# Kernel tuning notes

Hardware: AMD Instinct MI355X
Metric: run time of the kernel (lower is better)

The kernel has to match this reference:

```python
import jax, jax.numpy as jnp
import numpy as np

N = 8192
NFEAT = 512
NHID = 512
NCLASS = 8
EPS = 1e-9
ADJ_P = 0.01  # edge density


def setup_inputs() -> dict:
    key = jax.random.key(0)
    ks = jax.random.split(key, 16)
    adj = (jax.random.uniform(ks[0], (N, N)) < ADJ_P).astype(jnp.float32)
    x = jax.random.normal(ks[1], (N, NFEAT), dtype=jnp.float32)
    s_in = 1.0 / np.sqrt(NFEAT)
    s_h = 1.0 / np.sqrt(NHID)
    return {
        "adj": adj,
        "x": x,
        "gcn1_W": jax.random.normal(ks[2], (NFEAT, NHID), jnp.float32) * s_in,
        "gcn1_b": jnp.zeros((NHID,), jnp.float32),
        "Qw": jax.random.normal(ks[3], (NHID, NHID), jnp.float32) * s_h,
        "Qb": jnp.zeros((NHID,), jnp.float32),
        "Kw": jax.random.normal(ks[4], (NHID, NHID), jnp.float32) * s_h,
        "Kb": jnp.zeros((NHID,), jnp.float32),
        "Vw": jax.random.normal(ks[5], (NHID, NHID), jnp.float32) * s_h,
        "Vb": jnp.zeros((NHID,), jnp.float32),
        "ln_g": jnp.ones((NHID,), jnp.float32),
        "ln_b": jnp.zeros((NHID,), jnp.float32),
        "gcn2_W": jax.random.normal(ks[6], (NHID, NCLASS), jnp.float32) * s_h,
        "gcn2_b": jnp.zeros((NCLASS,), jnp.float32),
    }


def _gcn_norm(a):
    # symmetric degree normalization D^{-1/2} A D^{-1/2}, degrees = row sums
    d_inv_sqrt = jax.lax.rsqrt(a.sum(axis=1) + EPS)  # [N]
    return d_inv_sqrt[:, None] * a * d_inv_sqrt[None, :]


def _layer_norm(x, g, b):
    mu = x.mean(axis=-1, keepdims=True)
    var = x.var(axis=-1, keepdims=True)
    return (x - mu) * jax.lax.rsqrt(var + 1e-5) * g + b


def reference(adj, x, gcn1_W, gcn1_b, Qw, Qb, Kw, Kb, Vw, Vb, ln_g, ln_b, gcn2_W, gcn2_b):
    # GraphConvolution: adj @ (x W) + b, then ReLU
    h = jax.nn.relu(adj @ (x @ gcn1_W) + gcn1_b)  # [N, NHID]
    Qh = h @ Qw + Qb
    Kh = h @ Kw + Kb
    Vh = h @ Vw + Vb
    # adjacency-masked dense scores (multiplicative mask, as in original)
    A_tilde = adj * (Qh @ Kh.T)  # [N, N]
    attention = jax.nn.softmax(A_tilde, axis=1)
    X_tilde = _gcn_norm(attention) @ Vh  # [N, NHID]
    X_tilde = _layer_norm(X_tilde, ln_g, ln_b)
    z = adj @ (X_tilde @ gcn2_W) + gcn2_b  # [N, NCLASS]
    return jax.nn.softmax(z, axis=1)
```

## Files before the change

kernel.cpp:

```cpp
#include <hip/hip_runtime.h>
#include <math.h>

#define N_NODES 8192
#define NFEAT 512
#define NHID 512
#define NCLASS 8
#define RCAP 192
#define KB_SPLIT 1536
#define KA_SPLIT 1024
#define NSLICE 8

__device__ inline ushort f2bf(float f) {
  uint32_t u = __float_as_uint(f);
  uint32_t r = u + 0x7fffu + ((u >> 16) & 1u);
  return (ushort)(r >> 16);
}
__device__ inline float bf2f(ushort h) { return __uint_as_float(((uint32_t)h) << 16); }

__global__ __launch_bounds__(256) void build_ell(const float* __restrict__ adj,
                                                 int* __restrict__ colidx,
                                                 int* __restrict__ deg) {
  int row = blockIdx.x;
  __shared__ int cnt;
  __shared__ int cols[RCAP];
  if (threadIdx.x == 0) cnt = 0;
  __syncthreads();
  const float4* arow = (const float4*)(adj + (size_t)row * N_NODES);
  for (int i = threadIdx.x; i < N_NODES / 4; i += 256) {
    float4 v = arow[i];
    int base = i * 4;
    if (v.x > 0.5f) { int p = atomicAdd(&cnt, 1); if (p < RCAP) cols[p] = base; }
    if (v.y > 0.5f) { int p = atomicAdd(&cnt, 1); if (p < RCAP) cols[p] = base + 1; }
    if (v.z > 0.5f) { int p = atomicAdd(&cnt, 1); if (p < RCAP) cols[p] = base + 2; }
    if (v.w > 0.5f) { int p = atomicAdd(&cnt, 1); if (p < RCAP) cols[p] = base + 3; }
  }
  __syncthreads();
  int d = cnt < RCAP ? cnt : RCAP;
  if (threadIdx.x == 0) deg[row] = d;
  for (int i = threadIdx.x; i < d; i += 256) colidx[(size_t)row * RCAP + i] = cols[i];
}

__global__ void transpose512(const float* __restrict__ in, float* __restrict__ out) {
  __shared__ float tile[32][33];
  int x = blockIdx.x * 32 + threadIdx.x;
  int y0 = blockIdx.y * 32;
  for (int i = threadIdx.y; i < 32; i += 8)
    tile[i][threadIdx.x] = in[(size_t)(y0 + i) * 512 + x];
  __syncthreads();
  int xo = blockIdx.y * 32 + threadIdx.x;
  int yo0 = blockIdx.x * 32;
  for (int i = threadIdx.y; i < 32; i += 8)
    out[(size_t)(yo0 + i) * 512 + xo] = tile[threadIdx.x][i];
}

__global__ __launch_bounds__(256) void sgemm64x128(const float* __restrict__ A,
                                                   const float* __restrict__ B,
                                                   float* __restrict__ C,
                                                   int M, int Nn, int K, int ldc) {
  __shared__ float As[16][68];
  __shared__ float Bs[16][132];
  const int tid = threadIdx.x;
  const int bm = blockIdx.y * 64, bn = blockIdx.x * 128;
  const int tx = tid & 15, ty = tid >> 4;
  const int arow = tid >> 2, acol = (tid & 3) << 2;
  const int brow = tid >> 4, bcol = (tid & 15) << 2;
  float acc[4][8];
#pragma unroll
  for (int i = 0; i < 4; ++i)
#pragma unroll
    for (int j = 0; j < 8; ++j) acc[i][j] = 0.f;
  const float* Ap = A + (size_t)(bm + arow) * K + acol;
  const float* Bp = B + (size_t)brow * Nn + bn + bcol;
  float4 av = *(const float4*)(Ap);
  float4 bv0 = *(const float4*)(Bp);
  float4 bv1 = *(const float4*)(Bp + 64);
  for (int k0 = 0; k0 < K; k0 += 16) {
    if (k0) __syncthreads();
    As[acol + 0][arow] = av.x;
    As[acol + 1][arow] = av.y;
    As[acol + 2][arow] = av.z;
    As[acol + 3][arow] = av.w;
    *(float4*)&Bs[brow][bcol] = bv0;
    *(float4*)&Bs[brow][bcol + 64] = bv1;
    __syncthreads();
    int kn = (k0 + 16 < K) ? k0 + 16 : 0;
    av = *(const float4*)(Ap + kn);
    bv0 = *(const float4*)(Bp + (size_t)kn * Nn);
    bv1 = *(const float4*)(Bp + (size_t)kn * Nn + 64);
#pragma unroll
    for (int kk = 0; kk < 16; ++kk) {
      float4 a = *(const float4*)&As[kk][ty << 2];
      float4 b0 = *(const float4*)&Bs[kk][tx << 2];
      float4 b1 = *(const float4*)&Bs[kk][(tx << 2) + 64];
      float ar[4] = {a.x, a.y, a.z, a.w};
      float br[8] = {b0.x, b0.y, b0.z, b0.w, b1.x, b1.y, b1.z, b1.w};
#pragma unroll
      for (int i = 0; i < 4; ++i)
#pragma unroll
        for (int j = 0; j < 8; ++j) acc[i][j] = fmaf(ar[i], br[j], acc[i][j]);
    }
  }
#pragma unroll
  for (int i = 0; i < 4; ++i) {
    int r = bm + (ty << 2) + i;
    *(float4*)(C + (size_t)r * ldc + bn + (tx << 2)) =
        make_float4(acc[i][0], acc[i][1], acc[i][2], acc[i][3]);
    *(float4*)(C + (size_t)r * ldc + bn + 64 + (tx << 2)) =
        make_float4(acc[i][4], acc[i][5], acc[i][6], acc[i][7]);
  }
}

__global__ __launch_bounds__(256) void split_a2(const float* __restrict__ A, ushort* __restrict__ As) {
  int idx = blockIdx.x * 256 + threadIdx.x;
  int m = idx >> 7, t = idx & 127;
  float4 v = ((const float4*)(A + (size_t)m * 512))[t];
  ushort4 hi, lo;
  hi.x = f2bf(v.x); hi.y = f2bf(v.y); hi.z = f2bf(v.z); hi.w = f2bf(v.w);
  lo.x = f2bf(v.x - bf2f(hi.x)); lo.y = f2bf(v.y - bf2f(hi.y));
  lo.z = f2bf(v.z - bf2f(hi.z)); lo.w = f2bf(v.w - bf2f(hi.w));
  ushort* row = As + (size_t)m * KA_SPLIT;
  ((ushort4*)row)[t] = hi;
  ((ushort4*)(row + 512))[t] = lo;
}

__global__ __launch_bounds__(256) void split_bt(const float* __restrict__ B, ushort* __restrict__ Bt, int Nn) {
  int idx = blockIdx.x * 256 + threadIdx.x;
  int n = idx / 384, t = idx % 384;
  int sec = t >> 7;
  int k0 = (t & 127) << 2;
  ushort4 o;
  float f0 = B[(size_t)(k0 + 0) * Nn + n];
  float f1 = B[(size_t)(k0 + 1) * Nn + n];
  float f2 = B[(size_t)(k0 + 2) * Nn + n];
  float f3 = B[(size_t)(k0 + 3) * Nn + n];
  if (sec == 1) {
    o.x = f2bf(f0 - bf2f(f2bf(f0))); o.y = f2bf(f1 - bf2f(f2bf(f1)));
    o.z = f2bf(f2 - bf2f(f2bf(f2))); o.w = f2bf(f3 - bf2f(f2bf(f3)));
  } else {
    o.x = f2bf(f0); o.y = f2bf(f1); o.z = f2bf(f2); o.w = f2bf(f3);
  }
  ((ushort4*)(Bt + (size_t)n * KB_SPLIT))[t] = o;
}

__global__ __launch_bounds__(256) void split_bt_cat(const float* __restrict__ Mm, const float* __restrict__ Vw,
                                                    ushort* __restrict__ Bt) {
  int idx = blockIdx.x * 256 + threadIdx.x;
  int n = idx / 384, t = idx % 384;
  const float* src = (n < 512) ? (Mm + n) : (Vw + (n - 512));
  int sec = t >> 7;
  int k0 = (t & 127) << 2;
  ushort4 o;
  float f0 = src[(size_t)(k0 + 0) * 512];
  float f1 = src[(size_t)(k0 + 1) * 512];
  float f2 = src[(size_t)(k0 + 2) * 512];
  float f3 = src[(size_t)(k0 + 3) * 512];
  if (sec == 1) {
    o.x = f2bf(f0 - bf2f(f2bf(f0))); o.y = f2bf(f1 - bf2f(f2bf(f1)));
    o.z = f2bf(f2 - bf2f(f2bf(f2))); o.w = f2bf(f3 - bf2f(f2bf(f3)));
  } else {
    o.x = f2bf(f0); o.y = f2bf(f1); o.z = f2bf(f2); o.w = f2bf(f3);
  }
  ((ushort4*)(Bt + (size_t)n * KB_SPLIT))[t] = o;
}

__global__ void build_bcat(const float* __restrict__ Vb, float* __restrict__ bcat) {
  int i = blockIdx.x * 256 + threadIdx.x;
  bcat[i] = (i < 512) ? 0.f : Vb[i - 512];
}

using frag_ab = __attribute__((ext_vector_type(8))) short;
using frag_cd = __attribute__((ext_vector_type(4))) float;

__global__ __launch_bounds__(256) void mfma_gemm_bt(const ushort* __restrict__ A,
                                                    const ushort* __restrict__ Bt,
                                                    const float* __restrict__ bias,
                                                    float* __restrict__ C,
                                                    int ldc) {
  __shared__ __align__(16) ushort Atile[128 * 64];
  __shared__ __align__(16) ushort Btile[128 * 64];
  const int tid = threadIdx.x;
  const int w = tid >> 6, lane = tid & 63;
  const int m0 = blockIdx.y * 128, n0 = blockIdx.x * 128;
  const int wm = (w >> 1) * 64, wn = (w & 1) * 64;
  const int q = lane >> 4, c16 = lane & 15;

  frag_cd acc[4][4];
#pragma unroll
  for (int i = 0; i < 4; ++i)
#pragma unroll
    for (int j = 0; j < 4; ++j) acc[i][j] = (frag_cd){0.f, 0.f, 0.f, 0.f};

  const int srow = (w << 3) + (lane >> 3);
  const int scolb = (lane & 7) << 4;
  const uint8_t* gA = (const uint8_t*)A + (size_t)(m0 + srow) * (KA_SPLIT * 2) + scolb;
  const uint8_t* gB = (const uint8_t*)Bt + (size_t)(n0 + srow) * (KB_SPLIT * 2) + scolb;

  for (int c = 0; c < 24; ++c) {
    const size_t kaB = (size_t)((c < 8 ? c : c - 8) * 128);
    const size_t kbB = (size_t)(c * 128);
#pragma unroll
    for (int r = 0; r < 4; ++r) {
      __builtin_amdgcn_global_load_lds(
          (const __attribute__((address_space(1))) uint32_t*)(gA + (size_t)(r * 32) * (KA_SPLIT * 2) + kaB),
          (__attribute__((address_space(3))) uint32_t*)((uint8_t*)Atile + r * 4096 + w * 1024), 16, 0, 0);
      __builtin_amdgcn_global_load_lds(
          (const __attribute__((address_space(1))) uint32_t*)(gB + (size_t)(r * 32) * (KB_SPLIT * 2) + kbB),
          (__attribute__((address_space(3))) uint32_t*)((uint8_t*)Btile + r * 4096 + w * 1024), 16, 0, 0);
    }
    __syncthreads();
#pragma unroll
    for (int kk = 0; kk < 2; ++kk) {
      frag_ab af[4], bf[4];
#pragma unroll
      for (int i = 0; i < 4; ++i) {
        af[i] = *(const frag_ab*)((const uint8_t*)Atile + (wm + i * 16 + c16) * 128 + kk * 64 + q * 16);
        bf[i] = *(const frag_ab*)((const uint8_t*)Btile + (wn + i * 16 + c16) * 128 + kk * 64 + q * 16);
      }
#pragma unroll
      for (int i = 0; i < 4; ++i)
#pragma unroll
        for (int j = 0; j < 4; ++j)
          acc[i][j] = __builtin_amdgcn_mfma_f32_16x16x32_bf16(af[i], bf[j], acc[i][j], 0, 0, 0);
    }
    __syncthreads();
  }
#pragma unroll
  for (int j = 0; j < 4; ++j) {
    int col = n0 + wn + j * 16 + c16;
    float bv = bias ? bias[col] : 0.f;
#pragma unroll
    for (int i = 0; i < 4; ++i) {
      int row = m0 + wm + i * 16 + q * 4;
#pragma unroll
      for (int r = 0; r < 4; ++r)
        C[(size_t)(row + r) * ldc + col] = acc[i][j][r] + bv;
    }
  }
}

__global__ __launch_bounds__(64) void bias_prep(const float* __restrict__ Qw, const float* __restrict__ Kw,
                                                const float* __restrict__ Qb, const float* __restrict__ Kb,
                                                float* __restrict__ u, float* __restrict__ w,
                                                float* __restrict__ cbuf) {
  int k = blockIdx.x;
  int lane = threadIdx.x;
  if (k == NHID) {
    float s = 0.f;
    for (int j = lane; j < NHID; j += 64) s = fmaf(Qb[j], Kb[j], s);
#pragma unroll
    for (int o = 32; o > 0; o >>= 1) s += __shfl_down(s, o, 64);
    if (lane == 0) cbuf[0] = s;
    return;
  }
  float su = 0.f, sw = 0.f;
  for (int j = lane; j < NHID; j += 64) {
    su = fmaf(Qw[(size_t)k * NHID + j], Kb[j], su);
    sw = fmaf(Kw[(size_t)k * NHID + j], Qb[j], sw);
  }
#pragma unroll
  for (int o = 32; o > 0; o >>= 1) { su += __shfl_down(su, o, 64); sw += __shfl_down(sw, o, 64); }
  if (lane == 0) { u[k] = su; w[k] = sw; }
}

__global__ __launch_bounds__(128) void spmm_slice(const float* __restrict__ xW,
                                                  const int* __restrict__ colidx,
                                                  const int* __restrict__ deg,
                                                  float* __restrict__ h, int s0, int init) {
  int row = blockIdx.x;
  int d = deg[row];
  __shared__ int scols[RCAP];
  __shared__ int scnt;
  int t = threadIdx.x;
  if (t == 0) scnt = 0;
  __syncthreads();
  int klo = s0 << 10, khi = klo + 1024;
  for (int i = t; i < d; i += 128) {
    int c = colidx[(size_t)row * RCAP + i];
    if (c >= klo && c < khi) { int p = atomicAdd(&scnt, 1); scols[p] = c; }
  }
  __syncthreads();
  int n = scnt;
  float4 acc = init ? make_float4(0.f, 0.f, 0.f, 0.f) : ((float4*)(h + (size_t)row * NHID))[t];
  int e = 0;
  for (; e + 4 <= n; e += 4) {
    float4 v0 = ((const float4*)(xW + (size_t)scols[e + 0] * NHID))[t];
    float4 v1 = ((const float4*)(xW + (size_t)scols[e + 1] * NHID))[t];
    float4 v2 = ((const float4*)(xW + (size_t)scols[e + 2] * NHID))[t];
    float4 v3 = ((const float4*)(xW + (size_t)scols[e + 3] * NHID))[t];
    acc.x += (v0.x + v1.x) + (v2.x + v3.x);
    acc.y += (v0.y + v1.y) + (v2.y + v3.y);
    acc.z += (v0.z + v1.z) + (v2.z + v3.z);
    acc.w += (v0.w + v1.w) + (v2.w + v3.w);
  }
  for (; e < n; ++e) {
    float4 v = ((const float4*)(xW + (size_t)scols[e] * NHID))[t];
    acc.x += v.x; acc.y += v.y; acc.z += v.z; acc.w += v.w;
  }
  ((float4*)(h + (size_t)row * NHID))[t] = acc;
}

__global__ __launch_bounds__(128) void h_finalize(float* __restrict__ h, const float* __restrict__ b1,
                                                  const float* __restrict__ u, const float* __restrict__ w,
                                                  ushort* __restrict__ Hs, float* __restrict__ a_vec,
                                                  float* __restrict__ b_vec) {
  __shared__ float ra[2], rb[2];
  int row = blockIdx.x, t = threadIdx.x;
  int wv = t >> 6, lane = t & 63;
  float4 v = ((float4*)(h + (size_t)row * NHID))[t];
  float4 bv = ((const float4*)b1)[t];
  float4 o = make_float4(fmaxf(v.x + bv.x, 0.f), fmaxf(v.y + bv.y, 0.f),
                         fmaxf(v.z + bv.z, 0.f), fmaxf(v.w + bv.w, 0.f));
  ((float4*)(h + (size_t)row * NHID))[t] = o;
  ushort4 hi, lo;
  hi.x = f2bf(o.x); hi.y = f2bf(o.y); hi.z = f2bf(o.z); hi.w = f2bf(o.w);
  lo.x = f2bf(o.x - bf2f(hi.x)); lo.y = f2bf(o.y - bf2f(hi.y));
  lo.z = f2bf(o.z - bf2f(hi.z)); lo.w = f2bf(o.w - bf2f(hi.w));
  ushort* hr = Hs + (size_t)row * KA_SPLIT;
  ((ushort4*)hr)[t] = hi;
  ((ushort4*)(hr + 512))[t] = lo;
  float4 uv = ((const float4*)u)[t], wv4 = ((const float4*)w)[t];
  float sa = fmaf(o.x, uv.x, fmaf(o.y, uv.y, fmaf(o.z, uv.z, o.w * uv.w)));
  float sb = fmaf(o.x, wv4.x, fmaf(o.y, wv4.y, fmaf(o.z, wv4.z, o.w * wv4.w)));
#pragma unroll
  for (int off = 32; off > 0; off >>= 1) { sa += __shfl_down(sa, off, 64); sb += __shfl_down(sb, off, 64); }
  if (lane == 0) { ra[wv] = sa; rb[wv] = sb; }
  __syncthreads();
  if (t == 0) { a_vec[row] = ra[0] + ra[1]; b_vec[row] = rb[0] + rb[1]; }
}

__global__ __launch_bounds__(256) void score_slice(const float* __restrict__ G, int ldg,
                                                   const float* __restrict__ h,
                                                   const int* __restrict__ colidx,
                                                   const int* __restrict__ deg, int s0,
                                                   float* __restrict__ score) {
  __shared__ float gs[4][NHID];
  __shared__ int sel_e[4][RCAP];
  __shared__ int sel_c[4][RCAP];
  __shared__ int cnt[4];
  int t = threadIdx.x, wv = t >> 6, lane = t & 63;
  int row = blockIdx.x * 4 + wv;
  int d = deg[row];
  if (lane == 0) cnt[wv] = 0;
  __syncthreads();
  int klo = s0 << 10, khi = klo + 1024;
  for (int i = lane; i < d; i += 64) {
    int c = colidx[(size_t)row * RCAP + i];
    if (c >= klo && c < khi) { int p = atomicAdd(&cnt[wv], 1); sel_e[wv][p] = i; sel_c[wv][p] = c; }
  }
  const float4* gr = (const float4*)(G + (size_t)row * ldg);
  ((float4*)gs[wv])[lane] = gr[lane];
  ((float4*)gs[wv])[64 + lane] = gr[64 + lane];
  __syncthreads();
  int n = cnt[wv];
  int q = lane >> 4, u = lane & 15;
  const float4* gq = (const float4*)gs[wv] + u;
  for (int e0 = 0; e0 < n; e0 += 4) {
    int idx = e0 + q;
    bool act = idx < n;
    int col = sel_c[wv][act ? idx : 0];
    const float4* hr = (const float4*)(h + (size_t)col * NHID) + u;
    float s_a = 0.f, s_b = 0.f;
#pragma unroll
    for (int it = 0; it < 8; it += 2) {
      float4 h0 = hr[it * 16], g0 = gq[it * 16];
      float4 h1 = hr[(it + 1) * 16], g1 = gq[(it + 1) * 16];
      s_a = fmaf(h0.x, g0.x, s_a); s_a = fmaf(h0.y, g0.y, s_a);
      s_a = fmaf(h0.z, g0.z, s_a); s_a = fmaf(h0.w, g0.w, s_a);
      s_b = fmaf(h1.x, g1.x, s_b); s_b = fmaf(h1.y, g1.y, s_b);
      s_b = fmaf(h1.z, g1.z, s_b); s_b = fmaf(h1.w, g1.w, s_b);
    }
    float s = s_a + s_b;
    s += __shfl_down(s, 8, 16);
    s += __shfl_down(s, 4, 16);
    s += __shfl_down(s, 2, 16);
    s += __shfl_down(s, 1, 16);
    if (u == 0 && act) score[(size_t)row * RCAP + sel_e[wv][idx]] = s;
  }
}

__global__ void zero_vec(float* __restrict__ T) { T[threadIdx.x] = 0.f; }

__global__ __launch_bounds__(256) void colsum_atomic(const float* __restrict__ Vh, int ldv,
                                                     float* __restrict__ T) {
  int t = threadIdx.x;
  int r0 = blockIdx.x * 128;
  float2 s = make_float2(0.f, 0.f);
  for (int r = 0; r < 128; ++r) {
    float2 v = ((const float2*)(Vh + (size_t)(r0 + r) * ldv))[t];
    s.x += v.x;
    s.y += v.y;
  }
  atomicAdd(&T[2 * t], s.x);
  atomicAdd(&T[2 * t + 1], s.y);
}

__global__ __launch_bounds__(256) void softmax_agg_ln(const float* __restrict__ score,
                                                      const int* __restrict__ colidx, const int* __restrict__ deg,
                                                      const float* __restrict__ a_vec, const float* __restrict__ b_vec,
                                                      const float* __restrict__ cbuf,
                                                      const float* __restrict__ Vh, int ldv,
                                                      const float* __restrict__ T,
                                                      const float* __restrict__ lng, const float* __restrict__ lnb,
                                                      float* __restrict__ Xt) {
  __shared__ int scols[4][RCAP];
  __shared__ float sv[4][RCAP];
  int t = threadIdx.x, wv = t >> 6, lane = t & 63;
  int row = blockIdx.x * 4 + wv;
  int d = deg[row];
  float ai = a_vec[row] + cbuf[0];
  for (int i = lane; i < d; i += 64) {
    int c = colidx[(size_t)row * RCAP + i];
    scols[wv][i] = c;
    sv[wv][i] = score[(size_t)row * RCAP + i] + ai + b_vec[c];
  }
  __syncthreads();
  float m = 0.f;
  for (int i = lane; i < d; i += 64) m = fmaxf(m, sv[wv][i]);
#pragma unroll
  for (int o = 32; o > 0; o >>= 1) m = fmaxf(m, __shfl_xor(m, o, 64));
  float ssum = 0.f;
  for (int i = lane; i < d; i += 64) {
    float ex = expf(sv[wv][i] - m);
    sv[wv][i] = ex;
    ssum += ex;
  }
#pragma unroll
  for (int o = 32; o > 0; o >>= 1) ssum += __shfl_xor(ssum, o, 64);
  float em = expf(-m);
  float inv = 1.f / (ssum + (float)(N_NODES - d) * em);
  float ci = em * inv;
  __syncthreads();
  float4 a0 = make_float4(0.f, 0.f, 0.f, 0.f), a1 = a0;
  for (int e = 0; e < d; ++e) {
    float we = sv[wv][e] * inv;
    if (we > 1e-12f) {
      const float4* vr = (const float4*)(Vh + (size_t)scols[wv][e] * ldv);
      float4 v0 = vr[lane * 2], v1 = vr[lane * 2 + 1];
      a0.x = fmaf(we, v0.x, a0.x); a0.y = fmaf(we, v0.y, a0.y);
      a0.z = fmaf(we, v0.z, a0.z); a0.w = fmaf(we, v0.w, a0.w);
      a1.x = fmaf(we, v1.x, a1.x); a1.y = fmaf(we, v1.y, a1.y);
      a1.z = fmaf(we, v1.z, a1.z); a1.w = fmaf(we, v1.w, a1.w);
    }
  }
  float4 t0 = ((const float4*)T)[lane * 2], t1 = ((const float4*)T)[lane * 2 + 1];
  a0.x = fmaf(ci, t0.x, a0.x); a0.y = fmaf(ci, t0.y, a0.y);
  a0.z = fmaf(ci, t0.z, a0.z); a0.w = fmaf(ci, t0.w, a0.w);
  a1.x = fmaf(ci, t1.x, a1.x); a1.y = fmaf(ci, t1.y, a1.y);
  a1.z = fmaf(ci, t1.z, a1.z); a1.w = fmaf(ci, t1.w, a1.w);
  float s1 = ((a0.x + a0.y) + (a0.z + a0.w)) + ((a1.x + a1.y) + (a1.z + a1.w));
  float s2 = ((a0.x * a0.x + a0.y * a0.y) + (a0.z * a0.z + a0.w * a0.w)) +
             ((a1.x * a1.x + a1.y * a1.y) + (a1.z * a1.z + a1.w * a1.w));
#pragma unroll
  for (int o = 32; o > 0; o >>= 1) { s1 += __shfl_xor(s1, o, 64); s2 += __shfl_xor(s2, o, 64); }
  float mu = s1 * (1.f / NHID);
  float var = s2 * (1.f / NHID) - mu * mu;
  float rstd = rsqrtf(var + 1e-5f);
  float4 g0 = ((const float4*)lng)[lane * 2], g1 = ((const float4*)lng)[lane * 2 + 1];
  float4 b0 = ((const float4*)lnb)[lane * 2], b1 = ((const float4*)lnb)[lane * 2 + 1];
  float4 o0, o1;
  o0.x = (a0.x - mu) * rstd * g0.x + b0.x;
  o0.y = (a0.y - mu) * rstd * g0.y + b0.y;
  o0.z = (a0.z - mu) * rstd * g0.z + b0.z;
  o0.w = (a0.w - mu) * rstd * g0.w + b0.w;
  o1.x = (a1.x - mu) * rstd * g1.x + b1.x;
  o1.y = (a1.y - mu) * rstd * g1.y + b1.y;
  o1.z = (a1.z - mu) * rstd * g1.z + b1.z;
  o1.w = (a1.w - mu) * rstd * g1.w + b1.w;
  float4* xr = (float4*)(Xt + (size_t)row * NHID);
  xr[lane * 2] = o0;
  xr[lane * 2 + 1] = o1;
}

__global__ __launch_bounds__(256) void xt_w2(const float* __restrict__ Xt, const float* __restrict__ W2,
                                             float* __restrict__ Y) {
  __shared__ float w2s[NHID * NCLASS];
  int t = threadIdx.x;
  for (int i = t; i < NHID * NCLASS; i += 256) w2s[i] = W2[i];
  __syncthreads();
  int wv = t >> 6, lane = t & 63;
  int row = blockIdx.x * 4 + wv;
  const float4* xr = (const float4*)(Xt + (size_t)row * NHID);
  float4 x0 = xr[lane * 2], x1 = xr[lane * 2 + 1];
  float xv[8] = {x0.x, x0.y, x0.z, x0.w, x1.x, x1.y, x1.z, x1.w};
  float acc[NCLASS];
#pragma unroll
  for (int c = 0; c < NCLASS; ++c) acc[c] = 0.f;
#pragma unroll
  for (int kk = 0; kk < 8; ++kk) {
    int k = lane * 8 + kk;
#pragma unroll
    for (int c = 0; c < NCLASS; ++c) acc[c] = fmaf(xv[kk], w2s[k * NCLASS + c], acc[c]);
  }
#pragma unroll
  for (int c = 0; c < NCLASS; ++c)
#pragma unroll
    for (int o = 32; o > 0; o >>= 1) acc[c] += __shfl_down(acc[c], o, 64);
  if (lane == 0) {
    *(float4*)(Y + (size_t)row * NCLASS) = make_float4(acc[0], acc[1], acc[2], acc[3]);
    *(float4*)(Y + (size_t)row * NCLASS + 4) = make_float4(acc[4], acc[5], acc[6], acc[7]);
  }
}

__global__ __launch_bounds__(256) void final_spmm_softmax(const float* __restrict__ Y,
                                                          const int* __restrict__ colidx,
                                                          const int* __restrict__ deg,
                                                          const float* __restrict__ b2,
                                                          float* __restrict__ out) {
  int t = threadIdx.x;
  int wv = t >> 6, lane = t & 63;
  int row = blockIdx.x * 4 + wv;
  int d = deg[row];
  const int* cols = colidx + (size_t)row * RCAP;
  float acc[8];
#pragma unroll
  for (int c = 0; c < 8; ++c) acc[c] = 0.f;
  for (int e = lane; e < d; e += 64) {
    int col = cols[e];
    const float4* yr = (const float4*)(Y + (size_t)col * 8);
    float4 y0 = yr[0], y1 = yr[1];
    acc[0] += y0.x; acc[1] += y0.y; acc[2] += y0.z; acc[3] += y0.w;
    acc[4] += y1.x; acc[5] += y1.y; acc[6] += y1.z; acc[7] += y1.w;
  }
#pragma unroll
  for (int c = 0; c < 8; ++c)
#pragma unroll
    for (int o = 32; o > 0; o >>= 1) acc[c] += __shfl_down(acc[c], o, 64);
  if (lane == 0) {
    float z[8];
    float m = -1e30f;
#pragma unroll
    for (int c = 0; c < 8; ++c) { z[c] = acc[c] + b2[c]; m = fmaxf(m, z[c]); }
    float s = 0.f;
#pragma unroll
    for (int c = 0; c < 8; ++c) { z[c] = expf(z[c] - m); s += z[c]; }
    float inv = 1.f / s;
    *(float4*)(out + (size_t)row * 8) = make_float4(z[0] * inv, z[1] * inv, z[2] * inv, z[3] * inv);
    *(float4*)(out + (size_t)row * 8 + 4) = make_float4(z[4] * inv, z[5] * inv, z[6] * inv, z[7] * inv);
  }
}

extern "C" void kernel_launch(void* const* d_in, const int* in_sizes, int n_in,
                              void* d_out, int out_size, void* d_ws, size_t ws_size,
                              hipStream_t stream) {
  const float* adj = (const float*)d_in[0];
  const float* x = (const float*)d_in[1];
  const float* W1 = (const float*)d_in[2];
  const float* b1 = (const float*)d_in[3];
  const float* Qw = (const float*)d_in[4];
  const float* Qb = (const float*)d_in[5];
  const float* Kw = (const float*)d_in[6];
  const float* Kb = (const float*)d_in[7];
  const float* Vw = (const float*)d_in[8];
  const float* Vb = (const float*)d_in[9];
  const float* ln_g = (const float*)d_in[10];
  const float* ln_b = (const float*)d_in[11];
  const float* W2 = (const float*)d_in[12];
  const float* b2 = (const float*)d_in[13];
  float* out = (float*)d_out;

  char* ws = (char*)d_ws;
  size_t off = 0;
  auto alloc = [&](size_t bytes) -> void* {
    void* p = ws + off;
    off = (off + bytes + 255) & ~(size_t)255;
    return p;
  };
  int* colidx = (int*)alloc((size_t)N_NODES * RCAP * 4);
  int* deg = (int*)alloc((size_t)N_NODES * 4);
  float* bufA = (float*)alloc((size_t)N_NODES * NHID * 4);
  float* bufB = (float*)alloc((size_t)N_NODES * NHID * 4);
  float* GVh = (float*)alloc((size_t)N_NODES * 1024 * 4);
  ushort* Xs = (ushort*)alloc((size_t)N_NODES * KA_SPLIT * 2);
  ushort* Hs = (ushort*)alloc((size_t)N_NODES * KA_SPLIT * 2);
  ushort* W1ts = (ushort*)alloc((size_t)512 * KB_SPLIT * 2);
  ushort* Bcts = (ushort*)alloc((size_t)1024 * KB_SPLIT * 2);
  float* KwT = (float*)alloc((size_t)512 * 512 * 4);
  float* Mmat = (float*)alloc((size_t)512 * 512 * 4);
  float* bcat = (float*)alloc((size_t)1024 * 4);
  float* edge_s = (float*)alloc((size_t)N_NODES * RCAP * 4);
  float* a_vec = (float*)alloc((size_t)N_NODES * 4);
  float* b_vec = (float*)alloc((size_t)N_NODES * 4);
  float* u_vec = (float*)alloc((size_t)NHID * 4);
  float* w_vec = (float*)alloc((size_t)NHID * 4);
  float* cbuf = (float*)alloc(256);
  float* T = (float*)alloc((size_t)NHID * 4);
  float* Y = (float*)alloc((size_t)N_NODES * NCLASS * 4);
  (void)in_sizes; (void)n_in; (void)out_size; (void)ws_size;

  build_ell<<<N_NODES, 256, 0, stream>>>(adj, colidx, deg);
  transpose512<<<dim3(16, 16), dim3(32, 8), 0, stream>>>(Kw, KwT);
  bias_prep<<<NHID + 1, 64, 0, stream>>>(Qw, Kw, Qb, Kb, u_vec, w_vec, cbuf);
  sgemm64x128<<<dim3(4, 8), 256, 0, stream>>>(Qw, KwT, Mmat, 512, 512, 512, 512);
  split_a2<<<(N_NODES * 128) / 256, 256, 0, stream>>>(x, Xs);
  split_bt<<<(512 * 384) / 256, 256, 0, stream>>>(W1, W1ts, 512);
  mfma_gemm_bt<<<dim3(4, 64), 256, 0, stream>>>(Xs, W1ts, nullptr, bufA, 512);
  for (int s = 0; s < NSLICE; ++s)
    spmm_slice<<<N_NODES, 128, 0, stream>>>(bufA, colidx, deg, bufB, s, s == 0);
  h_finalize<<<N_NODES, 128, 0, stream>>>(bufB, b1, u_vec, w_vec, Hs, a_vec, b_vec);
  split_bt_cat<<<(1024 * 384) / 256, 256, 0, stream>>>(Mmat, Vw, Bcts);
  build_bcat<<<4, 256, 0, stream>>>(Vb, bcat);
  mfma_gemm_bt<<<dim3(8, 64), 256, 0, stream>>>(Hs, Bcts, bcat, GVh, 1024);
  zero_vec<<<1, 512, 0, stream>>>(T);
  colsum_atomic<<<64, 256, 0, stream>>>(GVh + 512, 1024, T);
  for (int s = 0; s < NSLICE; ++s)
    score_slice<<<N_NODES / 4, 256, 0, stream>>>(GVh, 1024, bufB, colidx, deg, s, edge_s);
  softmax_agg_ln<<<N_NODES / 4, 256, 0, stream>>>(edge_s, colidx, deg, a_vec, b_vec, cbuf,
                                                  GVh + 512, 1024, T, ln_g, ln_b, bufA);
  xt_w2<<<N_NODES / 4, 256, 0, stream>>>(bufA, W2, Y);
  final_spmm_softmax<<<N_NODES / 4, 256, 0, stream>>>(Y, colidx, deg, b2, out);
}
```

Measured before the change: 812.3 us.

## Fuse sliced SpMM and score passes into single kernels with per-block bucketing

Replaces the eight per-slice SpMM launches plus the finalize kernel with one fused kernel. It buckets each row's neighbours by column slice in shared memory and walks the slices in a rotated order, to keep the cache locality the slicing was meant to give. Likewise merges the eight score launches with the softmax/aggregate/LayerNorm kernel, dropping the edge score buffer round trip. The column sum of Vh moves into the GEMM epilogue as atomics. This cuts many launches and re-reads of colidx, but loses the global slice ordering across blocks, which may hurt L2 reuse. The bucket layout assumes at most 64 neighbours per slice.

```diff
diff --git a/kernel.cpp b/kernel.cpp
--- a/kernel.cpp
+++ b/kernel.cpp
@@ -8,7 +8,6 @@
 #define RCAP 192
 #define KB_SPLIT 1536
 #define KA_SPLIT 1024
-#define NSLICE 8
 
 __device__ inline ushort f2bf(float f) {
   uint32_t u = __float_as_uint(f);
@@ -175,7 +174,7 @@
                                                     const ushort* __restrict__ Bt,
                                                     const float* __restrict__ bias,
                                                     float* __restrict__ C,
-                                                    int ldc) {
+                                                    int ldc, float* __restrict__ Tsum) {
   __shared__ __align__(16) ushort Atile[128 * 64];
   __shared__ __align__(16) ushort Btile[128 * 64];
   const int tid = threadIdx.x;
@@ -228,12 +227,21 @@
   for (int j = 0; j < 4; ++j) {
     int col = n0 + wn + j * 16 + c16;
     float bv = bias ? bias[col] : 0.f;
+    float csum = 0.f;
 #pragma unroll
     for (int i = 0; i < 4; ++i) {
       int row = m0 + wm + i * 16 + q * 4;
 #pragma unroll
-      for (int r = 0; r < 4; ++r)
-        C[(size_t)(row + r) * ldc + col] = acc[i][j][r] + bv;
+      for (int r = 0; r < 4; ++r) {
+        float v = acc[i][j][r] + bv;
+        C[(size_t)(row + r) * ldc + col] = v;
+        csum += v;
+      }
+    }
+    if (Tsum && col >= 512) {
+      csum += __shfl_xor(csum, 16, 64);
+      csum += __shfl_xor(csum, 32, 64);
+      if (q == 0) atomicAdd(&Tsum[col - 512], csum);
     }
   }
 }
@@ -262,54 +270,52 @@
   if (lane == 0) { u[k] = su; w[k] = sw; }
 }
 
-__global__ __launch_bounds__(128) void spmm_slice(const float* __restrict__ xW,
+__global__ __launch_bounds__(128) void spmm_fused(const float* __restrict__ xW,
                                                   const int* __restrict__ colidx,
                                                   const int* __restrict__ deg,
-                                                  float* __restrict__ h, int s0, int init) {
-  int row = blockIdx.x;
+                                                  const float* __restrict__ b1,
+                                                  const float* __restrict__ u, const float* __restrict__ w,
+                                                  float* __restrict__ h, ushort* __restrict__ Hs,
+                                                  float* __restrict__ a_vec, float* __restrict__ b_vec) {
+  __shared__ int bls[512];
+  __shared__ int bcnt[8];
+  __shared__ float ra[2], rb[2];
+  int row = blockIdx.x, t = threadIdx.x;
   int d = deg[row];
-  __shared__ int scols[RCAP];
-  __shared__ int scnt;
-  int t = threadIdx.x;
-  if (t == 0) scnt = 0;
-  __syncthreads();
-  int klo = s0 << 10, khi = klo + 1024;
+  if (t < 8) bcnt[t] = 0;
+  __syncthreads();
   for (int i = t; i < d; i += 128) {
     int c = colidx[(size_t)row * RCAP + i];
-    if (c >= klo && c < khi) { int p = atomicAdd(&scnt, 1); scols[p] = c; }
-  }
-  __syncthreads();
-  int n = scnt;
-  float4 acc = init ? make_float4(0.f, 0.f, 0.f, 0.f) : ((float4*)(h + (size_t)row * NHID))[t];
-  int e = 0;
-  for (; e + 4 <= n; e += 4) {
-    float4 v0 = ((const float4*)(xW + (size_t)scols[e + 0] * NHID))[t];
-    float4 v1 = ((const float4*)(xW + (size_t)scols[e + 1] * NHID))[t];
-    float4 v2 = ((const float4*)(xW + (size_t)scols[e + 2] * NHID))[t];
-    float4 v3 = ((const float4*)(xW + (size_t)scols[e + 3] * NHID))[t];
-    acc.x += (v0.x + v1.x) + (v2.x + v3.x);
-    acc.y += (v0.y + v1.y) + (v2.y + v3.y);
-    acc.z += (v0.z + v1.z) + (v2.z + v3.z);
-    acc.w += (v0.w + v1.w) + (v2.w + v3.w);
-  }
-  for (; e < n; ++e) {
-    float4 v = ((const float4*)(xW + (size_t)scols[e] * NHID))[t];
-    acc.x += v.x; acc.y += v.y; acc.z += v.z; acc.w += v.w;
-  }
-  ((float4*)(h + (size_t)row * NHID))[t] = acc;
-}
-
-__global__ __launch_bounds__(128) void h_finalize(float* __restrict__ h, const float* __restrict__ b1,
-                                                  const float* __restrict__ u, const float* __restrict__ w,
-                                                  ushort* __restrict__ Hs, float* __restrict__ a_vec,
-                                                  float* __restrict__ b_vec) {
-  __shared__ float ra[2], rb[2];
-  int row = blockIdx.x, t = threadIdx.x;
-  int wv = t >> 6, lane = t & 63;
-  float4 v = ((float4*)(h + (size_t)row * NHID))[t];
+    int s = c >> 10;
+    int p = atomicAdd(&bcnt[s], 1);
+    bls[(s << 6) | p] = c;
+  }
+  __syncthreads();
+  float4 acc = make_float4(0.f, 0.f, 0.f, 0.f);
+  int xcd = blockIdx.x & 7;
+  for (int k = 0; k < 8; ++k) {
+    int s = (xcd + k) & 7;
+    int n = bcnt[s];
+    const int* bp = &bls[s << 6];
+    int e = 0;
+    for (; e + 4 <= n; e += 4) {
+      float4 v0 = ((const float4*)(xW + (size_t)bp[e + 0] * NHID))[t];
+      float4 v1 = ((const float4*)(xW + (size_t)bp[e + 1] * NHID))[t];
+      float4 v2 = ((const float4*)(xW + (size_t)bp[e + 2] * NHID))[t];
+      float4 v3 = ((const float4*)(xW + (size_t)bp[e + 3] * NHID))[t];
+      acc.x += (v0.x + v1.x) + (v2.x + v3.x);
+      acc.y += (v0.y + v1.y) + (v2.y + v3.y);
+      acc.z += (v0.z + v1.z) + (v2.z + v3.z);
+      acc.w += (v0.w + v1.w) + (v2.w + v3.w);
+    }
+    for (; e < n; ++e) {
+      float4 v = ((const float4*)(xW + (size_t)bp[e] * NHID))[t];
+      acc.x += v.x; acc.y += v.y; acc.z += v.z; acc.w += v.w;
+    }
+  }
   float4 bv = ((const float4*)b1)[t];
-  float4 o = make_float4(fmaxf(v.x + bv.x, 0.f), fmaxf(v.y + bv.y, 0.f),
-                         fmaxf(v.z + bv.z, 0.f), fmaxf(v.w + bv.w, 0.f));
+  float4 o = make_float4(fmaxf(acc.x + bv.x, 0.f), fmaxf(acc.y + bv.y, 0.f),
+                         fmaxf(acc.z + bv.z, 0.f), fmaxf(acc.w + bv.w, 0.f));
   ((float4*)(h + (size_t)row * NHID))[t] = o;
   ushort4 hi, lo;
   hi.x = f2bf(o.x); hi.y = f2bf(o.y); hi.z = f2bf(o.z); hi.w = f2bf(o.w);
@@ -321,6 +327,7 @@
   float4 uv = ((const float4*)u)[t], wv4 = ((const float4*)w)[t];
   float sa = fmaf(o.x, uv.x, fmaf(o.y, uv.y, fmaf(o.z, uv.z, o.w * uv.w)));
   float sb = fmaf(o.x, wv4.x, fmaf(o.y, wv4.y, fmaf(o.z, wv4.z, o.w * wv4.w)));
+  int wv = t >> 6, lane = t & 63;
 #pragma unroll
   for (int off = 32; off > 0; off >>= 1) { sa += __shfl_down(sa, off, 64); sb += __shfl_down(sb, off, 64); }
   if (lane == 0) { ra[wv] = sa; rb[wv] = sb; }
@@ -328,90 +335,66 @@
   if (t == 0) { a_vec[row] = ra[0] + ra[1]; b_vec[row] = rb[0] + rb[1]; }
 }
 
-__global__ __launch_bounds__(256) void score_slice(const float* __restrict__ G, int ldg,
-                                                   const float* __restrict__ h,
-                                                   const int* __restrict__ colidx,
-                                                   const int* __restrict__ deg, int s0,
-                                                   float* __restrict__ score) {
+__global__ void zero_vec(float* __restrict__ T) { T[threadIdx.x] = 0.f; }
+
+__global__ __launch_bounds__(256) void score_softmax_agg_ln(
+    const float* __restrict__ G, int ldg, const float* __restrict__ h,
+    const int* __restrict__ colidx, const int* __restrict__ deg,
+    const float* __restrict__ a_vec, const float* __restrict__ b_vec,
+    const float* __restrict__ cbuf, const float* __restrict__ Vh, int ldv,
+    const float* __restrict__ T, const float* __restrict__ lng,
+    const float* __restrict__ lnb, float* __restrict__ Xt) {
   __shared__ float gs[4][NHID];
-  __shared__ int sel_e[4][RCAP];
-  __shared__ int sel_c[4][RCAP];
-  __shared__ int cnt[4];
-  int t = threadIdx.x, wv = t >> 6, lane = t & 63;
-  int row = blockIdx.x * 4 + wv;
-  int d = deg[row];
-  if (lane == 0) cnt[wv] = 0;
-  __syncthreads();
-  int klo = s0 << 10, khi = klo + 1024;
-  for (int i = lane; i < d; i += 64) {
-    int c = colidx[(size_t)row * RCAP + i];
-    if (c >= klo && c < khi) { int p = atomicAdd(&cnt[wv], 1); sel_e[wv][p] = i; sel_c[wv][p] = c; }
-  }
-  const float4* gr = (const float4*)(G + (size_t)row * ldg);
-  ((float4*)gs[wv])[lane] = gr[lane];
-  ((float4*)gs[wv])[64 + lane] = gr[64 + lane];
-  __syncthreads();
-  int n = cnt[wv];
-  int q = lane >> 4, u = lane & 15;
-  const float4* gq = (const float4*)gs[wv] + u;
-  for (int e0 = 0; e0 < n; e0 += 4) {
-    int idx = e0 + q;
-    bool act = idx < n;
-    int col = sel_c[wv][act ? idx : 0];
-    const float4* hr = (const float4*)(h + (size_t)col * NHID) + u;
-    float s_a = 0.f, s_b = 0.f;
-#pragma unroll
-    for (int it = 0; it < 8; it += 2) {
-      float4 h0 = hr[it * 16], g0 = gq[it * 16];
-      float4 h1 = hr[(it + 1) * 16], g1 = gq[(it + 1) * 16];
-      s_a = fmaf(h0.x, g0.x, s_a); s_a = fmaf(h0.y, g0.y, s_a);
-      s_a = fmaf(h0.z, g0.z, s_a); s_a = fmaf(h0.w, g0.w, s_a);
-      s_b = fmaf(h1.x, g1.x, s_b); s_b = fmaf(h1.y, g1.y, s_b);
-      s_b = fmaf(h1.z, g1.z, s_b); s_b = fmaf(h1.w, g1.w, s_b);
-    }
-    float s = s_a + s_b;
-    s += __shfl_down(s, 8, 16);
-    s += __shfl_down(s, 4, 16);
-    s += __shfl_down(s, 2, 16);
-    s += __shfl_down(s, 1, 16);
-    if (u == 0 && act) score[(size_t)row * RCAP + sel_e[wv][idx]] = s;
-  }
-}
-
-__global__ void zero_vec(float* __restrict__ T) { T[threadIdx.x] = 0.f; }
-
-__global__ __launch_bounds__(256) void colsum_atomic(const float* __restrict__ Vh, int ldv,
-                                                     float* __restrict__ T) {
-  int t = threadIdx.x;
-  int r0 = blockIdx.x * 128;
-  float2 s = make_float2(0.f, 0.f);
-  for (int r = 0; r < 128; ++r) {
-    float2 v = ((const float2*)(Vh + (size_t)(r0 + r) * ldv))[t];
-    s.x += v.x;
-    s.y += v.y;
-  }
-  atomicAdd(&T[2 * t], s.x);
-  atomicAdd(&T[2 * t + 1], s.y);
-}
-
-__global__ __launch_bounds__(256) void softmax_agg_ln(const float* __restrict__ score,
-                                                      const int* __restrict__ colidx, const int* __restrict__ deg,
-                                                      const float* __restrict__ a_vec, const float* __restrict__ b_vec,
-                                                      const float* __restrict__ cbuf,
-                                                      const float* __restrict__ Vh, int ldv,
-                                                      const float* __restrict__ T,
-                                                      const float* __restrict__ lng, const float* __restrict__ lnb,
-                                                      float* __restrict__ Xt) {
+  __shared__ int bls[4][512];
+  __shared__ int bcnt[4][8];
   __shared__ int scols[4][RCAP];
   __shared__ float sv[4][RCAP];
   int t = threadIdx.x, wv = t >> 6, lane = t & 63;
   int row = blockIdx.x * 4 + wv;
   int d = deg[row];
-  float ai = a_vec[row] + cbuf[0];
+  if (lane < 8) bcnt[wv][lane] = 0;
+  const float4* gr = (const float4*)(G + (size_t)row * ldg);
+  ((float4*)gs[wv])[lane] = gr[lane];
+  ((float4*)gs[wv])[64 + lane] = gr[64 + lane];
+  __syncthreads();
   for (int i = lane; i < d; i += 64) {
     int c = colidx[(size_t)row * RCAP + i];
     scols[wv][i] = c;
-    sv[wv][i] = score[(size_t)row * RCAP + i] + ai + b_vec[c];
+    int s = c >> 10;
+    int p = atomicAdd(&bcnt[wv][s], 1);
+    bls[wv][(s << 6) | p] = (c << 8) | i;
+  }
+  __syncthreads();
+  float ai = a_vec[row] + cbuf[0];
+  int xcd = blockIdx.x & 7;
+  int q = lane >> 4, u = lane & 15;
+  const float4* gq = (const float4*)gs[wv] + u;
+  for (int k = 0; k < 8; ++k) {
+    int s = (xcd + k) & 7;
+    int n = bcnt[wv][s];
+    for (int e0 = 0; e0 < n; e0 += 4) {
+      int idx = e0 + q;
+      bool act = idx < n;
+      int pack = bls[wv][(s << 6) | (act ? idx : 0)];
+      int col = pack >> 8;
+      const float4* hr = (const float4*)(h + (size_t)col * NHID) + u;
+      float s_a = 0.f, s_b = 0.f;
+#pragma unroll
+      for (int it = 0; it < 8; it += 2) {
+        float4 h0 = hr[it * 16], g0 = gq[it * 16];
+        float4 h1 = hr[(it + 1) * 16], g1 = gq[(it + 1) * 16];
+        s_a = fmaf(h0.x, g0.x, s_a); s_a = fmaf(h0.y, g0.y, s_a);
+        s_a = fmaf(h0.z, g0.z, s_a); s_a = fmaf(h0.w, g0.w, s_a);
+        s_b = fmaf(h1.x, g1.x, s_b); s_b = fmaf(h1.y, g1.y, s_b);
+        s_b = fmaf(h1.z, g1.z, s_b); s_b = fmaf(h1.w, g1.w, s_b);
+      }
+      float sc = s_a + s_b;
+      sc += __shfl_down(sc, 8, 16);
+      sc += __shfl_down(sc, 4, 16);
+      sc += __shfl_down(sc, 2, 16);
+      sc += __shfl_down(sc, 1, 16);
+      if (u == 0 && act) sv[wv][pack & 255] = sc + ai + b_vec[col];
+    }
   }
   __syncthreads();
   float m = 0.f;
@@ -577,7 +560,6 @@
   float* KwT = (float*)alloc((size_t)512 * 512 * 4);
   float* Mmat = (float*)alloc((size_t)512 * 512 * 4);
   float* bcat = (float*)alloc((size_t)1024 * 4);
-  float* edge_s = (float*)alloc((size_t)N_NODES * RCAP * 4);
   float* a_vec = (float*)alloc((size_t)N_NODES * 4);
   float* b_vec = (float*)alloc((size_t)N_NODES * 4);
   float* u_vec = (float*)alloc((size_t)NHID * 4);
@@ -593,19 +575,14 @@
   sgemm64x128<<<dim3(4, 8), 256, 0, stream>>>(Qw, KwT, Mmat, 512, 512, 512, 512);
   split_a2<<<(N_NODES * 128) / 256, 256, 0, stream>>>(x, Xs);
   split_bt<<<(512 * 384) / 256, 256, 0, stream>>>(W1, W1ts, 512);
-  mfma_gemm_bt<<<dim3(4, 64), 256, 0, stream>>>(Xs, W1ts, nullptr, bufA, 512);
-  for (int s = 0; s < NSLICE; ++s)
-    spmm_slice<<<N_NODES, 128, 0, stream>>>(bufA, colidx, deg, bufB, s, s == 0);
-  h_finalize<<<N_NODES, 128, 0, stream>>>(bufB, b1, u_vec, w_vec, Hs, a_vec, b_vec);
+  mfma_gemm_bt<<<dim3(4, 64), 256, 0, stream>>>(Xs, W1ts, nullptr, bufA, 512, nullptr);
+  spmm_fused<<<N_NODES, 128, 0, stream>>>(bufA, colidx, deg, b1, u_vec, w_vec, bufB, Hs, a_vec, b_vec);
   split_bt_cat<<<(1024 * 384) / 256, 256, 0, stream>>>(Mmat, Vw, Bcts);
   build_bcat<<<4, 256, 0, stream>>>(Vb, bcat);
-  mfma_gemm_bt<<<dim3(8, 64), 256, 0, stream>>>(Hs, Bcts, bcat, GVh, 1024);
   zero_vec<<<1, 512, 0, stream>>>(T);
-  colsum_atomic<<<64, 256, 0, stream>>>(GVh + 512, 1024, T);
-  for (int s = 0; s < NSLICE; ++s)
-    score_slice<<<N_NODES / 4, 256, 0, stream>>>(GVh, 1024, bufB, colidx, deg, s, edge_s);
-  softmax_agg_ln<<<N_NODES / 4, 256, 0, stream>>>(edge_s, colidx, deg, a_vec, b_vec, cbuf,
-                                                  GVh + 512, 1024, T, ln_g, ln_b, bufA);
+  mfma_gemm_bt<<<dim3(8, 64), 256, 0, stream>>>(Hs, Bcts, bcat, GVh, 1024, T);
+  score_softmax_agg_ln<<<N_NODES / 4, 256, 0, stream>>>(GVh, 1024, bufB, colidx, deg, a_vec, b_vec,
+                                                        cbuf, GVh + 512, 1024, T, ln_g, ln_b, bufA);
   xt_w2<<<N_NODES / 4, 256, 0, stream>>>(bufA, W2, Y);
   final_spmm_softmax<<<N_NODES / 4, 256, 0, stream>>>(Y, colidx, deg, b2, out);
 }
```

Result: no change. 803.3 us (-1.1%).
